# Kernel tuning notes

Measured on AMD Instinct MI355X. Metric: run time of the kernel, lower is better.

The kernel has to match this reference:

```python
import jax, jax.numpy as jnp
import numpy as np

B, LT, LC, D, H = 128, 64, 400, 768, 3072  # batch, template len, search len, dim, mlp hidden
NEG = -1e20


def _l2norm(x):
    # F.normalize(dim=-1): x / max(||x||, eps)
    n = jnp.sqrt(jnp.sum(x * x, axis=-1, keepdims=True))
    return x / jnp.maximum(n, 1e-12)


def setup_inputs() -> dict:
    key = jax.random.key(0)
    ks = jax.random.split(key, 10)
    tem = jax.random.normal(ks[0], (B, LT, D), jnp.float32)
    ctx = jax.random.normal(ks[1], (B, LC, D), jnp.float32)
    cls_token = jax.random.normal(ks[2], (B, D), jnp.float32)
    tem_mask = jax.random.randint(ks[3], (B, LT), 0, 2) > 0
    ctx_mask = jax.random.randint(ks[4], (B, LC), 0, 2) > 0
    flag = jax.random.randint(ks[5], (B,), 0, 3)
    query_embed = jax.random.normal(ks[6], (3, D), jnp.float32) * 0.02
    logit_scale = jnp.asarray(np.log(1.0 / 0.07), jnp.float32)
    fc1_w = jax.random.normal(ks[7], (D, H), jnp.float32) * 0.02
    fc1_b = jnp.zeros((H,), jnp.float32)
    fc2_w = jax.random.normal(ks[8], (H, D), jnp.float32) * 0.02
    fc2_b = jnp.zeros((D,), jnp.float32)
    return dict(tem=tem, tem_mask=tem_mask, ctx=ctx, ctx_mask=ctx_mask,
                cls_token=cls_token, flag=flag, query_embed=query_embed,
                logit_scale=logit_scale, fc1_w=fc1_w, fc1_b=fc1_b,
                fc2_w=fc2_w, fc2_b=fc2_b)


def _divide_background(bgd_score):
    # sort ascending, cumsum threshold at 0.25, keep scores >= threshold
    values = jnp.sort(bgd_score, axis=-1)
    mask = jnp.cumsum(values, axis=-1) < 0.25
    threshold = jnp.min(jnp.where(mask, 1.0, values), axis=-1, keepdims=True)
    return bgd_score >= threshold


def _forward(tem, ctx, cls_token, query_embed, logit_scale,
             fc1_w, fc1_b, fc2_w, fc2_b, tem_mask, ctx_mask, flag):
    b = tem.shape[0]
    src_ = jnp.tile(query_embed[None], (b, 1, 1)).at[:, 0].add(cls_token)  # [B,3,D]
    tgt = jnp.concatenate([tem, ctx], axis=1)                               # [B,L,D]
    tgt_mask = jnp.concatenate([tem_mask, ctx_mask], axis=1)[:, None, :]    # [B,1,L]
    sim_logit = jnp.einsum('bd,bld->bl', _l2norm(cls_token), _l2norm(tgt))[:, None, :]
    sim_logit = sim_logit * jnp.exp(logit_scale)                            # [B,1,L]

    tgt_score = jax.nn.softmax(jnp.where(tgt_mask, sim_logit, NEG), axis=-1)
    tgt_token = tgt_score @ tgt                                             # [B,1,D]
    bgd_logit = jnp.where(tgt_mask, NEG, sim_logit)
    bgd_score0 = jax.nn.softmax(bgd_logit, axis=-1)
    dis_mask = _divide_background(bgd_score0)
    bgd_score = jax.nn.softmax(jnp.where(dis_mask, NEG, bgd_logit), axis=-1)
    dis_score = jax.nn.softmax(jnp.where(dis_mask, bgd_logit, NEG), axis=-1)
    bgd_token = bgd_score @ tgt
    dis_token = dis_score @ tgt

    src = jnp.concatenate([tgt_token, dis_token, bgd_token], axis=1) + src_  # [B,3,D]
    h = jax.nn.gelu(src @ fc1_w + fc1_b, approximate=False)
    src = (h @ fc2_w + fc2_b) + src
    # stack [src, src_, src] and pick per-sample by flag
    stacked = jnp.stack([src, src_, src], axis=1)                            # [B,3,3,D]
    out = jnp.take_along_axis(stacked, flag[:, None, None, None], axis=1)[:, 0]
    return out  # [B,3,D]


def reference(tem, tem_mask, ctx, ctx_mask, cls_token, flag, query_embed,
              logit_scale, fc1_w, fc1_b, fc2_w, fc2_b):
    return _forward(tem, ctx, cls_token, query_embed, logit_scale,
                    fc1_w, fc1_b, fc2_w, fc2_b, tem_mask, ctx_mask, flag)
```

## Files before the change

kernel.cpp:

```cpp
#include <hip/hip_runtime.h>
#include <hip/hip_bf16.h>
#include <math.h>

typedef unsigned short u16;
typedef unsigned int   u32;
typedef unsigned char  u8;

#define NB  128
#define NLT 64
#define NLC 400
#define NL  464
#define ND  768
#define NH  3072
#define NEGF (-1e20f)

typedef __attribute__((ext_vector_type(8))) short bf16x8;
typedef __attribute__((ext_vector_type(4))) float f32x4;

__device__ __forceinline__ float b2f(u16 u){ return __uint_as_float(((u32)u)<<16); }
__device__ __forceinline__ u16 f2b(float f){
  u32 x = __float_as_uint(f);
  x += 0x7fffu + ((x>>16)&1u);
  return (u16)(x>>16);
}
template<bool BF> __device__ __forceinline__ float ldf(const void* p, size_t i){
  if constexpr (BF) return b2f(((const u16*)p)[i]);
  else              return ((const float*)p)[i];
}

__device__ __forceinline__ void detect_inline(const void* tem, const void* tmask,
                                              int* sh2, int& bf, int& m8){
  int tid = threadIdx.x;
  if (tid < 64){
    const u16* p = (const u16*)tem;
    float acc = 0.f;
    for (int i = tid; i < 512; i += 64){
      float v = fabsf(b2f(p[i]));
      acc += fminf(v, 1e10f);
    }
    for (int o = 32; o; o >>= 1) acc += __shfl_down(acc, o);
    const u8* mb = (const u8*)tmask;
    int nz = 0;
    for (int i = tid; i < 400; i += 64) if ((i & 3) != 0 && mb[i] != 0) nz = 1;
    unsigned long long anym = __ballot(nz);
    if (tid == 0){ sh2[0] = (acc < 1e4f) ? 1 : 0; sh2[1] = anym ? 1 : 0; }
  }
  __syncthreads();
  bf = sh2[0]; m8 = sh2[1];
}

__global__ __launch_bounds__(256) void k_prep(const void* tem, const void* tmask,
    const void* w1, const void* w2, u16* __restrict__ w1t, u16* __restrict__ w2t,
    int* flags){
  __shared__ int sh2[2];
  __shared__ u16 tile[64][66];
  int bf, m8;
  detect_inline(tem, tmask, sh2, bf, m8);
  if (blockIdx.x == 0 && blockIdx.y == 0 && threadIdx.x == 0){
    flags[0] = bf; flags[1] = m8;
  }
  int which = blockIdx.y;
  const void* W = which ? w2 : w1;
  u16* Wt = which ? w2t : w1t;
  int K = which ? NH : ND;
  int N = which ? ND : NH;
  int nt = N >> 6;
  int tk = blockIdx.x / nt, tn = blockIdx.x - tk*nt;
  int k0 = tk*64, n0 = tn*64;
  int r = threadIdx.x >> 6, c = threadIdx.x & 63;
  #pragma unroll
  for (int i = 0; i < 16; i++){
    int row = i*4 + r;
    size_t idx = (size_t)(k0 + row)*N + n0 + c;
    tile[row][c] = bf ? ((const u16*)W)[idx] : f2b(((const float*)W)[idx]);
  }
  __syncthreads();
  #pragma unroll
  for (int i = 0; i < 16; i++){
    int nrow = i*4 + r;
    Wt[(size_t)(n0 + nrow)*K + k0 + c] = tile[c][nrow];
  }
}

template<bool BF>
__device__ void sim_body(const void* tem, const void* ctx, const void* cls,
                         const void* lsp, float* sim,
                         float* clsf, float* red4, float* cnorm)
{
  int b = blockIdx.x, tile = blockIdx.y, tid = threadIdx.x;
  for (int i = tid; i < ND; i += 256) clsf[i] = ldf<BF>(cls, (size_t)b*ND + i);
  __syncthreads();
  float ss = 0.f;
  for (int i = tid; i < ND; i += 256) ss += clsf[i]*clsf[i];
  for (int off = 32; off; off >>= 1) ss += __shfl_down(ss, off);
  if ((tid & 63) == 0) red4[tid >> 6] = ss;
  __syncthreads();
  if (tid == 0) *cnorm = fmaxf(sqrtf(red4[0]+red4[1]+red4[2]+red4[3]), 1e-12f);
  __syncthreads();
  float cn = *cnorm;
  float escale = expf(ldf<BF>(lsp, 0));
  int lane = tid & 63, w = tid >> 6;
  float creg[12];
  #pragma unroll
  for (int j = 0; j < 12; j++) creg[j] = clsf[lane*12 + j];

  for (int rr = 0; rr < 4; rr++){
    int l = tile*16 + w + rr*4;
    float v[12];
    if constexpr (BF){
      const u16* row = (l < NLT) ? ((const u16*)tem + ((size_t)b*NLT + l)*ND)
                                 : ((const u16*)ctx + ((size_t)b*NLC + (l-NLT))*ND);
      const ushort4* rp = (const ushort4*)(row + lane*12);
      #pragma unroll
      for (int q = 0; q < 3; q++){
        ushort4 u = rp[q];
        v[q*4+0]=b2f(u.x); v[q*4+1]=b2f(u.y); v[q*4+2]=b2f(u.z); v[q*4+3]=b2f(u.w);
      }
    } else {
      const float* row = (l < NLT) ? ((const float*)tem + ((size_t)b*NLT + l)*ND)
                                   : ((const float*)ctx + ((size_t)b*NLC + (l-NLT))*ND);
      const float4* rp = (const float4*)(row + lane*12);
      #pragma unroll
      for (int q = 0; q < 3; q++){
        float4 u = rp[q];
        v[q*4+0]=u.x; v[q*4+1]=u.y; v[q*4+2]=u.z; v[q*4+3]=u.w;
      }
    }
    float dot = 0.f, rs = 0.f;
    #pragma unroll
    for (int j = 0; j < 12; j++){ dot += creg[j]*v[j]; rs += v[j]*v[j]; }
    for (int off = 32; off; off >>= 1){
      dot += __shfl_down(dot, off); rs += __shfl_down(rs, off);
    }
    if (lane == 0){
      float rn = fmaxf(sqrtf(rs), 1e-12f);
      sim[(size_t)b*NL + l] = dot / (cn*rn) * escale;
    }
  }
}
__global__ __launch_bounds__(256) void k_sim(const int* flags, const void* tem,
    const void* ctx, const void* cls, const void* lsp, float* sim){
  __shared__ float clsf[ND];
  __shared__ float red4[4];
  __shared__ float cnorm;
  if (flags[0]) sim_body<true >(tem, ctx, cls, lsp, sim, clsf, red4, &cnorm);
  else          sim_body<false>(tem, ctx, cls, lsp, sim, clsf, red4, &cnorm);
}

__device__ __forceinline__ float bsum512(float v, float* l8, int tid){
  #pragma unroll
  for (int o = 32; o; o >>= 1) v += __shfl_xor(v, o);
  __syncthreads();
  if ((tid & 63) == 0) l8[tid >> 6] = v;
  __syncthreads();
  float s = l8[0];
  #pragma unroll
  for (int i = 1; i < 8; i++) s += l8[i];
  return s;
}
__device__ __forceinline__ float bmax512(float v, float* l8, int tid){
  #pragma unroll
  for (int o = 32; o; o >>= 1) v = fmaxf(v, __shfl_xor(v, o));
  __syncthreads();
  if ((tid & 63) == 0) l8[tid >> 6] = v;
  __syncthreads();
  float s = l8[0];
  #pragma unroll
  for (int i = 1; i < 8; i++) s = fmaxf(s, l8[i]);
  return s;
}
__device__ __forceinline__ float bmin512(float v, float* l8, int tid){
  #pragma unroll
  for (int o = 32; o; o >>= 1) v = fminf(v, __shfl_xor(v, o));
  __syncthreads();
  if ((tid & 63) == 0) l8[tid >> 6] = v;
  __syncthreads();
  float s = l8[0];
  #pragma unroll
  for (int i = 1; i < 8; i++) s = fminf(s, l8[i]);
  return s;
}

template<bool M8>
__device__ void scores_body(const float* sim, const void* tmask, const void* cmask,
                            float* tgts, float* diss, float* bgds,
                            float* srt, float* wsum, float* l8)
{
  int b = blockIdx.x, tid = threadIdx.x;
  int lane = tid & 63, wid = tid >> 6;
  bool valid = tid < NL;
  float sv = valid ? sim[(size_t)b*NL + tid] : 0.f;
  bool mk = false;
  if (valid){
    if constexpr (M8)
      mk = (tid < NLT) ? (((const u8*)tmask)[b*NLT + tid] != 0)
                       : (((const u8*)cmask)[b*NLC + tid - NLT] != 0);
    else
      mk = (tid < NLT) ? (((const int*)tmask)[b*NLT + tid] != 0)
                       : (((const int*)cmask)[b*NLC + tid - NLT] != 0);
  }
  float lt = (valid && mk) ? sv : NEGF;
  float m1 = bmax512(lt, l8, tid);
  float e1 = valid ? expf(lt - m1) : 0.f;
  float s1 = bsum512(e1, l8, tid);
  if (valid) tgts[(size_t)b*NL + tid] = e1/s1;

  float bl = (valid && !mk) ? sv : NEGF;
  float m2 = bmax512(bl, l8, tid);
  float e2 = valid ? expf(bl - m2) : 0.f;
  float s2 = bsum512(e2, l8, tid);
  float bg0 = e2/s2;

  float v = valid ? bg0 : INFINITY;
  for (int k = 2; k <= 512; k <<= 1){
    for (int j = k >> 1; j >= 64; j >>= 1){
      __syncthreads();
      srt[tid] = v;
      __syncthreads();
      float p = srt[tid ^ j];
      bool up = ((tid & k) == 0), lower = ((tid & j) == 0);
      v = (up == lower) ? fminf(v, p) : fmaxf(v, p);
    }
    int j0 = (k >> 1) < 32 ? (k >> 1) : 32;
    for (int j = j0; j >= 1; j >>= 1){
      float p = __shfl_xor(v, j);
      bool up = ((tid & k) == 0), lower = ((tid & j) == 0);
      v = (up == lower) ? fminf(v, p) : fmaxf(v, p);
    }
  }
  float c = v;
  #pragma unroll
  for (int o = 1; o < 64; o <<= 1){
    float t = __shfl_up(c, o);
    if (lane >= o) c += t;
  }
  __syncthreads();
  if (lane == 63) wsum[wid] = c;
  __syncthreads();
  float off = 0.f;
  for (int i = 0; i < wid; i++) off += wsum[i];
  c += off;
  float cand = (c < 0.25f) ? 1.0f : v;
  float thr = bmin512(cand, l8, tid);

  bool dm = valid && (bg0 >= thr);
  float dl = dm ? bl : NEGF;
  float l2 = dm ? NEGF : bl;
  float m3 = bmax512(dl, l8, tid);
  float e3 = valid ? expf(dl - m3) : 0.f;
  float s3 = bsum512(e3, l8, tid);
  if (valid) diss[(size_t)b*NL + tid] = e3/s3;
  float m4 = bmax512(l2, l8, tid);
  float e4 = valid ? expf(l2 - m4) : 0.f;
  float s4 = bsum512(e4, l8, tid);
  if (valid) bgds[(size_t)b*NL + tid] = e4/s4;
}
__global__ __launch_bounds__(512) void k_scores(const int* flags, const float* sim,
    const void* tmask, const void* cmask, float* tgts, float* diss, float* bgds){
  __shared__ float srt[512];
  __shared__ float wsum[8];
  __shared__ float l8[8];
  if (flags[1]) scores_body<true >(sim, tmask, cmask, tgts, diss, bgds, srt, wsum, l8);
  else          scores_body<false>(sim, tmask, cmask, tgts, diss, bgds, srt, wsum, l8);
}

template<bool BF>
__device__ void tok_body(const void* tem, const void* ctx, const void* cls, const void* qe,
                         const float* __restrict__ tgts, const float* __restrict__ diss,
                         const float* __restrict__ bgds,
                         float* __restrict__ src0f, u16* __restrict__ src0b,
                         float (*ws)[NL], float (*red)[3][264])
{
  int b = blockIdx.x, dc = blockIdx.y, tid = threadIdx.x;
  int g = tid >> 5, l32 = tid & 31;
  int c0 = dc*256 + l32*8;
  for (int i = tid; i < NL; i += 256){
    ws[0][i] = tgts[(size_t)b*NL + i];
    ws[1][i] = diss[(size_t)b*NL + i];
    ws[2][i] = bgds[(size_t)b*NL + i];
  }
  __syncthreads();
  float acc[3][8];
  #pragma unroll
  for (int j = 0; j < 3; j++)
    #pragma unroll
    for (int q = 0; q < 8; q++) acc[j][q] = 0.f;

  for (int it = 0; it < 58; it++){
    int l = it*8 + g;
    float f[8];
    if constexpr (BF){
      const u16* row = (l < NLT) ? ((const u16*)tem + ((size_t)b*NLT + l)*ND)
                                 : ((const u16*)ctx + ((size_t)b*NLC + (l-NLT))*ND);
      uint4 v = *(const uint4*)(row + c0);
      f[0]=b2f((u16)(v.x&0xffff)); f[1]=b2f((u16)(v.x>>16));
      f[2]=b2f((u16)(v.y&0xffff)); f[3]=b2f((u16)(v.y>>16));
      f[4]=b2f((u16)(v.z&0xffff)); f[5]=b2f((u16)(v.z>>16));
      f[6]=b2f((u16)(v.w&0xffff)); f[7]=b2f((u16)(v.w>>16));
    } else {
      const float* row = (l < NLT) ? ((const float*)tem + ((size_t)b*NLT + l)*ND)
                                   : ((const float*)ctx + ((size_t)b*NLC + (l-NLT))*ND);
      float4 v0 = *(const float4*)(row + c0);
      float4 v1 = *(const float4*)(row + c0 + 4);
      f[0]=v0.x; f[1]=v0.y; f[2]=v0.z; f[3]=v0.w;
      f[4]=v1.x; f[5]=v1.y; f[6]=v1.z; f[7]=v1.w;
    }
    float w0 = ws[0][l], w1 = ws[1][l], w2 = ws[2][l];
    #pragma unroll
    for (int q = 0; q < 8; q++){
      acc[0][q] = fmaf(w0, f[q], acc[0][q]);
      acc[1][q] = fmaf(w1, f[q], acc[1][q]);
      acc[2][q] = fmaf(w2, f[q], acc[2][q]);
    }
  }
  #pragma unroll
  for (int j = 0; j < 3; j++)
    #pragma unroll
    for (int q = 0; q < 8; q++) red[g][j][l32*8 + q] = acc[j][q];
  __syncthreads();
  int col = dc*256 + tid;
  #pragma unroll
  for (int j = 0; j < 3; j++){
    float s = 0.f;
    #pragma unroll
    for (int g2 = 0; g2 < 8; g2++) s += red[g2][j][tid];
    s += ldf<BF>(qe, (size_t)j*ND + col);
    if (j == 0) s += ldf<BF>(cls, (size_t)b*ND + col);
    size_t oi = ((size_t)b*3 + j)*ND + col;
    src0f[oi] = s;
    src0b[oi] = f2b(s);
  }
}
__global__ __launch_bounds__(256) void k_tok(const int* flags, const void* tem,
    const void* ctx, const void* cls, const void* qe,
    const float* tgts, const float* diss, const float* bgds,
    float* src0f, u16* src0b){
  __shared__ float ws[3][NL];
  __shared__ float red[8][3][264];
  if (flags[0]) tok_body<true >(tem, ctx, cls, qe, tgts, diss, bgds, src0f, src0b, ws, red);
  else          tok_body<false>(tem, ctx, cls, qe, tgts, diss, bgds, src0f, src0b, ws, red);
}

__device__ __forceinline__ void mfma_loop2(const u16* __restrict__ A, int lda,
                                           const u16* __restrict__ B, int ldb,
                                           int m0, int n0, int kb_, int ke_,
                                           u16* lds, f32x4 (&acc)[2][2])
{
  int tid = threadIdx.x, lane = tid & 63;
  int w = tid >> 6, wr = w >> 1, wc = w & 1;
  #pragma unroll
  for (int i = 0; i < 2; i++)
    #pragma unroll
    for (int j = 0; j < 2; j++) acc[i][j] = (f32x4){0.f,0.f,0.f,0.f};

  int rS = tid >> 2, kcS = (tid & 3) * 16;
  uint4 a0, a1, b0, b1;
  auto LOAD = [&](int k0){
    const uint4* pa = (const uint4*)(A + (size_t)(m0 + rS)*lda + k0 + kcS);
    a0 = pa[0]; a1 = pa[1];
    const uint4* pb = (const uint4*)(B + (size_t)(n0 + rS)*ldb + k0 + kcS);
    b0 = pb[0]; b1 = pb[1];
  };
  auto WRITE = [&](u16* L){
    u32 sw = (u32)((rS & 7) << 4);
    u32 ba = (u32)(rS*128 + kcS*2);
    *(uint4*)((char*)L + (ba ^ sw)) = a0;
    *(uint4*)((char*)L + ((ba + 16) ^ sw)) = a1;
    *(uint4*)((char*)L + 8192 + (ba ^ sw)) = b0;
    *(uint4*)((char*)L + 8192 + ((ba + 16) ^ sw)) = b1;
  };

  int nt = (ke_ - kb_) >> 6;
  LOAD(kb_);
  WRITE(lds);
  __syncthreads();
  int cur = 0;
  for (int t = 0; t < nt; t++){
    if (t + 1 < nt) LOAD(kb_ + (t+1)*64);
    u16* L = lds + (size_t)cur*8192;
    #pragma unroll
    for (int kb = 0; kb < 2; kb++){
      bf16x8 af[2], bfr[2];
      #pragma unroll
      for (int i = 0; i < 2; i++){
        int ml = wr*32 + i*16 + (lane & 15);
        u32 ab = (u32)(ml*128 + kb*64 + (lane >> 4)*16) ^ (u32)((ml & 7) << 4);
        af[i] = *(const bf16x8*)((char*)L + ab);
        int cl = wc*32 + i*16 + (lane & 15);
        u32 bb = (u32)(cl*128 + kb*64 + (lane >> 4)*16) ^ (u32)((cl & 7) << 4);
        bfr[i] = *(const bf16x8*)((char*)L + 8192 + bb);
      }
      #pragma unroll
      for (int i = 0; i < 2; i++)
        #pragma unroll
        for (int j = 0; j < 2; j++)
          acc[i][j] = __builtin_amdgcn_mfma_f32_16x16x32_bf16(af[i], bfr[j], acc[i][j], 0, 0, 0);
    }
    if (t + 1 < nt) WRITE(lds + (size_t)(cur^1)*8192);
    __syncthreads();
    cur ^= 1;
  }
}

template<bool BF>
__device__ void fc1_body(const u16* src0b, const u16* w1t, const void* b1, u16* hbf, u16* lds){
  int n0 = blockIdx.x*64, m0 = blockIdx.y*64;
  f32x4 acc[2][2];
  mfma_loop2(src0b, ND, w1t, ND, m0, n0, 0, ND, lds, acc);
  int lane = threadIdx.x & 63, w = threadIdx.x >> 6, wr = w >> 1, wc = w & 1;
  #pragma unroll
  for (int j = 0; j < 2; j++){
    int n = n0 + wc*32 + j*16 + (lane & 15);
    float bb = ldf<BF>(b1, n);
    #pragma unroll
    for (int i = 0; i < 2; i++){
      int mb = m0 + wr*32 + i*16 + (lane >> 4)*4;
      #pragma unroll
      for (int r = 0; r < 4; r++){
        float x = acc[i][j][r] + bb;
        float g = 0.5f*x*(1.0f + erff(x*0.70710678118654752f));
        hbf[(size_t)(mb + r)*NH + n] = f2b(g);
      }
    }
  }
}
__global__ __launch_bounds__(256) void k_fc1(const int* flags, const u16* src0b,
    const u16* w1t, const void* b1, u16* hbf){
  __shared__ u16 lds[16384];
  if (flags[0]) fc1_body<true >(src0b, w1t, b1, hbf, lds);
  else          fc1_body<false>(src0b, w1t, b1, hbf, lds);
}

__global__ __launch_bounds__(256) void k_fc2(const int* flags, const u16* hbf,
    const u16* w2t, float* fc2p){
  __shared__ u16 lds[16384];
  int n0 = blockIdx.x*64, m0 = blockIdx.y*64, z = blockIdx.z;
  f32x4 acc[2][2];
  mfma_loop2(hbf, NH, w2t, NH, m0, n0, z*768, (z+1)*768, lds, acc);
  int lane = threadIdx.x & 63, w = threadIdx.x >> 6, wr = w >> 1, wc = w & 1;
  float* po = fc2p + (size_t)z*(384*ND);
  #pragma unroll
  for (int j = 0; j < 2; j++){
    int n = n0 + wc*32 + j*16 + (lane & 15);
    #pragma unroll
    for (int i = 0; i < 2; i++){
      int mb = m0 + wr*32 + i*16 + (lane >> 4)*4;
      #pragma unroll
      for (int r = 0; r < 4; r++)
        po[(size_t)(mb + r)*ND + n] = acc[i][j][r];
    }
  }
}

template<bool BF>
__device__ void fin_body(const float* __restrict__ p, const void* b2,
                         const float* __restrict__ src0f, const void* cls,
                         const void* qe, const int* flag, void* out){
  int idx = (blockIdx.x*256 + threadIdx.x)*4;
  int r = idx / ND;
  int n = idx % ND;
  float s[4] = {0,0,0,0};
  #pragma unroll
  for (int ksp = 0; ksp < 4; ksp++){
    float4 v = *(const float4*)(p + (size_t)ksp*(384*ND) + idx);
    s[0]+=v.x; s[1]+=v.y; s[2]+=v.z; s[3]+=v.w;
  }
  float4 res = *(const float4*)(src0f + idx);
  const float* rp = &res.x;
  int bi = r/3, j = r - bi*3;
  bool take_src_ = (flag[bi] == 1);
  #pragma unroll
  for (int jj = 0; jj < 4; jj++){
    float val = s[jj] + ldf<BF>(b2, n + jj) + rp[jj];
    if (take_src_){
      val = ldf<BF>(qe, (size_t)j*ND + n + jj)
          + ((j == 0) ? ldf<BF>(cls, (size_t)bi*ND + n + jj) : 0.f);
    }
    s[jj] = val;
  }
  if constexpr (BF){
    ushort4 o = { f2b(s[0]), f2b(s[1]), f2b(s[2]), f2b(s[3]) };
    *(ushort4*)((u16*)out + idx) = o;
  } else {
    float4 o = {s[0], s[1], s[2], s[3]};
    *(float4*)((float*)out + idx) = o;
  }
}
__global__ __launch_bounds__(256) void k_fin(const int* flags, const float* p,
    const void* b2, const float* src0f, const void* cls, const void* qe,
    const int* flag, void* out){
  if (flags[0]) fin_body<true >(p, b2, src0f, cls, qe, flag, out);
  else          fin_body<false>(p, b2, src0f, cls, qe, flag, out);
}

extern "C" void kernel_launch(void* const* d_in, const int* in_sizes, int n_in,
                              void* d_out, int out_size, void* d_ws, size_t ws_size,
                              hipStream_t stream)
{
  const void* tem   = d_in[0];
  const void* tmask = d_in[1];
  const void* ctx   = d_in[2];
  const void* cmask = d_in[3];
  const void* cls   = d_in[4];
  const int*  flag  = (const int*)d_in[5];
  const void* qe    = d_in[6];
  const void* ls    = d_in[7];
  const void* w1    = d_in[8];
  const void* b1    = d_in[9];
  const void* w2    = d_in[10];
  const void* b2    = d_in[11];

  int*   flags = (int*)d_ws;
  float* p     = (float*)d_ws + 16;
  float* sim   = p;  p += (size_t)NB*NL;
  float* tgts  = p;  p += (size_t)NB*NL;
  float* diss  = p;  p += (size_t)NB*NL;
  float* bgds  = p;  p += (size_t)NB*NL;
  float* src0f = p;  p += (size_t)384*ND;
  u16*   src0b = (u16*)p; p += (size_t)384*ND/2;
  u16*   hbf   = (u16*)p; p += (size_t)384*NH/2;
  float* fc2p  = p;  p += (size_t)4*384*ND;
  u16*   w1t   = (u16*)p; p += (size_t)ND*NH/2;
  u16*   w2t   = (u16*)p; p += (size_t)ND*NH/2;

  hipLaunchKernelGGL(k_prep,   dim3(576, 2), dim3(256), 0, stream,
                     tem, tmask, w1, w2, w1t, w2t, flags);
  hipLaunchKernelGGL(k_sim,    dim3(NB, 29), dim3(256), 0, stream, flags, tem, ctx, cls, ls, sim);
  hipLaunchKernelGGL(k_scores, dim3(NB), dim3(512), 0, stream, flags, sim, tmask, cmask, tgts, diss, bgds);
  hipLaunchKernelGGL(k_tok,    dim3(NB, 3), dim3(256), 0, stream,
                     flags, tem, ctx, cls, qe, tgts, diss, bgds, src0f, src0b);
  hipLaunchKernelGGL(k_fc1,    dim3(NH/64, 384/64), dim3(256), 0, stream, flags, src0b, w1t, b1, hbf);
  hipLaunchKernelGGL(k_fc2,    dim3(ND/64, 384/64, 4), dim3(256), 0, stream, flags, hbf, w2t, fc2p);
  hipLaunchKernelGGL(k_fin,    dim3(384*ND/1024), dim3(256), 0, stream,
                     flags, fc2p, b2, src0f, cls, qe, flag, d_out);
}
```

Before: 106.9 us.

## Fuse weight prep into sim kernel and stage bf16 copy of tgt for token pass

Merges the weight-transpose kernel and the similarity kernel into one launch with a flat grid, so both run concurrently and one launch is saved. In the fp32 path, the similarity pass also writes a bf16 copy of the concatenated tem/ctx rows, which the token-pooling kernel then reads instead of re-reading the fp32 inputs. This halves the bytes read in the token pass but adds an extra bf16 write of the whole tgt tensor and drops precision of the pooled tokens to bf16. The fused kernel also carries extra shared memory, which may lower occupancy.

```diff
diff --git a/kernel.cpp b/kernel.cpp
--- a/kernel.cpp
+++ b/kernel.cpp
@@ -49,45 +49,13 @@
   bf = sh2[0]; m8 = sh2[1];
 }
 
-__global__ __launch_bounds__(256) void k_prep(const void* tem, const void* tmask,
-    const void* w1, const void* w2, u16* __restrict__ w1t, u16* __restrict__ w2t,
-    int* flags){
-  __shared__ int sh2[2];
-  __shared__ u16 tile[64][66];
-  int bf, m8;
-  detect_inline(tem, tmask, sh2, bf, m8);
-  if (blockIdx.x == 0 && blockIdx.y == 0 && threadIdx.x == 0){
-    flags[0] = bf; flags[1] = m8;
-  }
-  int which = blockIdx.y;
-  const void* W = which ? w2 : w1;
-  u16* Wt = which ? w2t : w1t;
-  int K = which ? NH : ND;
-  int N = which ? ND : NH;
-  int nt = N >> 6;
-  int tk = blockIdx.x / nt, tn = blockIdx.x - tk*nt;
-  int k0 = tk*64, n0 = tn*64;
-  int r = threadIdx.x >> 6, c = threadIdx.x & 63;
-  #pragma unroll
-  for (int i = 0; i < 16; i++){
-    int row = i*4 + r;
-    size_t idx = (size_t)(k0 + row)*N + n0 + c;
-    tile[row][c] = bf ? ((const u16*)W)[idx] : f2b(((const float*)W)[idx]);
-  }
-  __syncthreads();
-  #pragma unroll
-  for (int i = 0; i < 16; i++){
-    int nrow = i*4 + r;
-    Wt[(size_t)(n0 + nrow)*K + k0 + c] = tile[c][nrow];
-  }
-}
-
 template<bool BF>
 __device__ void sim_body(const void* tem, const void* ctx, const void* cls,
-                         const void* lsp, float* sim,
+                         const void* lsp, float* sim, u16* __restrict__ tgtb,
+                         int b, int tile,
                          float* clsf, float* red4, float* cnorm)
 {
-  int b = blockIdx.x, tile = blockIdx.y, tid = threadIdx.x;
+  int tid = threadIdx.x;
   for (int i = tid; i < ND; i += 256) clsf[i] = ldf<BF>(cls, (size_t)b*ND + i);
   __syncthreads();
   float ss = 0.f;
@@ -125,6 +93,13 @@
         float4 u = rp[q];
         v[q*4+0]=u.x; v[q*4+1]=u.y; v[q*4+2]=u.z; v[q*4+3]=u.w;
       }
+      u16* orow = tgtb + ((size_t)b*NL + l)*ND + lane*12;
+      ushort4 s0 = { f2b(v[0]), f2b(v[1]), f2b(v[2]),  f2b(v[3]) };
+      ushort4 s1 = { f2b(v[4]), f2b(v[5]), f2b(v[6]),  f2b(v[7]) };
+      ushort4 s2 = { f2b(v[8]), f2b(v[9]), f2b(v[10]), f2b(v[11]) };
+      *(ushort4*)(orow + 0) = s0;
+      *(ushort4*)(orow + 4) = s1;
+      *(ushort4*)(orow + 8) = s2;
     }
     float dot = 0.f, rs = 0.f;
     #pragma unroll
@@ -138,13 +113,51 @@
     }
   }
 }
-__global__ __launch_bounds__(256) void k_sim(const int* flags, const void* tem,
-    const void* ctx, const void* cls, const void* lsp, float* sim){
+
+__global__ __launch_bounds__(256) void k_presim(const void* tem, const void* tmask,
+    const void* ctx, const void* cls, const void* lsp,
+    const void* w1, const void* w2, u16* __restrict__ w1t, u16* __restrict__ w2t,
+    float* sim, u16* tgtb, int* flags)
+{
+  __shared__ int sh2[2];
+  __shared__ u16 tile[64][66];
   __shared__ float clsf[ND];
   __shared__ float red4[4];
   __shared__ float cnorm;
-  if (flags[0]) sim_body<true >(tem, ctx, cls, lsp, sim, clsf, red4, &cnorm);
-  else          sim_body<false>(tem, ctx, cls, lsp, sim, clsf, red4, &cnorm);
+  int bf, m8;
+  detect_inline(tem, tmask, sh2, bf, m8);
+  int bid = blockIdx.x;
+  if (bid == 0 && threadIdx.x == 0){ flags[0] = bf; flags[1] = m8; }
+
+  if (bid < 1152){
+    int which = (bid >= 576) ? 1 : 0;
+    int t = which ? bid - 576 : bid;
+    const void* W = which ? w2 : w1;
+    u16* Wt = which ? w2t : w1t;
+    int K = which ? NH : ND;
+    int N = which ? ND : NH;
+    int nt = N >> 6;
+    int tk = t / nt, tn = t - tk*nt;
+    int k0 = tk*64, n0 = tn*64;
+    int r = threadIdx.x >> 6, c = threadIdx.x & 63;
+    #pragma unroll
+    for (int i = 0; i < 16; i++){
+      int row = i*4 + r;
+      size_t idx = (size_t)(k0 + row)*N + n0 + c;
+      tile[row][c] = bf ? ((const u16*)W)[idx] : f2b(((const float*)W)[idx]);
+    }
+    __syncthreads();
+    #pragma unroll
+    for (int i = 0; i < 16; i++){
+      int nrow = i*4 + r;
+      Wt[(size_t)(n0 + nrow)*K + k0 + c] = tile[c][nrow];
+    }
+  } else {
+    int sid = bid - 1152;
+    int b = sid / 29, tl = sid - b*29;
+    if (bf) sim_body<true >(tem, ctx, cls, lsp, sim, tgtb, b, tl, clsf, red4, &cnorm);
+    else    sim_body<false>(tem, ctx, cls, lsp, sim, tgtb, b, tl, clsf, red4, &cnorm);
+  }
 }
 
 __device__ __forceinline__ float bsum512(float v, float* l8, int tid){
@@ -265,7 +278,8 @@
 }
 
 template<bool BF>
-__device__ void tok_body(const void* tem, const void* ctx, const void* cls, const void* qe,
+__device__ void tok_body(const void* tem, const void* ctx, const u16* __restrict__ tgtb,
+                         const void* cls, const void* qe,
                          const float* __restrict__ tgts, const float* __restrict__ diss,
                          const float* __restrict__ bgds,
                          float* __restrict__ src0f, u16* __restrict__ src0b,
@@ -288,23 +302,19 @@
 
   for (int it = 0; it < 58; it++){
     int l = it*8 + g;
+    const u16* row;
+    if constexpr (BF){
+      row = (l < NLT) ? ((const u16*)tem + ((size_t)b*NLT + l)*ND)
+                      : ((const u16*)ctx + ((size_t)b*NLC + (l-NLT))*ND);
+    } else {
+      row = tgtb + ((size_t)b*NL + l)*ND;
+    }
+    uint4 v = *(const uint4*)(row + c0);
     float f[8];
-    if constexpr (BF){
-      const u16* row = (l < NLT) ? ((const u16*)tem + ((size_t)b*NLT + l)*ND)
-                                 : ((const u16*)ctx + ((size_t)b*NLC + (l-NLT))*ND);
-      uint4 v = *(const uint4*)(row + c0);
-      f[0]=b2f((u16)(v.x&0xffff)); f[1]=b2f((u16)(v.x>>16));
-      f[2]=b2f((u16)(v.y&0xffff)); f[3]=b2f((u16)(v.y>>16));
-      f[4]=b2f((u16)(v.z&0xffff)); f[5]=b2f((u16)(v.z>>16));
-      f[6]=b2f((u16)(v.w&0xffff)); f[7]=b2f((u16)(v.w>>16));
-    } else {
-      const float* row = (l < NLT) ? ((const float*)tem + ((size_t)b*NLT + l)*ND)
-                                   : ((const float*)ctx + ((size_t)b*NLC + (l-NLT))*ND);
-      float4 v0 = *(const float4*)(row + c0);
-      float4 v1 = *(const float4*)(row + c0 + 4);
-      f[0]=v0.x; f[1]=v0.y; f[2]=v0.z; f[3]=v0.w;
-      f[4]=v1.x; f[5]=v1.y; f[6]=v1.z; f[7]=v1.w;
-    }
+    f[0]=b2f((u16)(v.x&0xffff)); f[1]=b2f((u16)(v.x>>16));
+    f[2]=b2f((u16)(v.y&0xffff)); f[3]=b2f((u16)(v.y>>16));
+    f[4]=b2f((u16)(v.z&0xffff)); f[5]=b2f((u16)(v.z>>16));
+    f[6]=b2f((u16)(v.w&0xffff)); f[7]=b2f((u16)(v.w>>16));
     float w0 = ws[0][l], w1 = ws[1][l], w2 = ws[2][l];
     #pragma unroll
     for (int q = 0; q < 8; q++){
@@ -332,13 +342,13 @@
   }
 }
 __global__ __launch_bounds__(256) void k_tok(const int* flags, const void* tem,
-    const void* ctx, const void* cls, const void* qe,
+    const void* ctx, const u16* tgtb, const void* cls, const void* qe,
     const float* tgts, const float* diss, const float* bgds,
     float* src0f, u16* src0b){
   __shared__ float ws[3][NL];
   __shared__ float red[8][3][264];
-  if (flags[0]) tok_body<true >(tem, ctx, cls, qe, tgts, diss, bgds, src0f, src0b, ws, red);
-  else          tok_body<false>(tem, ctx, cls, qe, tgts, diss, bgds, src0f, src0b, ws, red);
+  if (flags[0]) tok_body<true >(tem, ctx, tgtb, cls, qe, tgts, diss, bgds, src0f, src0b, ws, red);
+  else          tok_body<false>(tem, ctx, tgtb, cls, qe, tgts, diss, bgds, src0f, src0b, ws, red);
 }
 
 __device__ __forceinline__ void mfma_loop2(const u16* __restrict__ A, int lda,
@@ -522,13 +532,13 @@
   float* fc2p  = p;  p += (size_t)4*384*ND;
   u16*   w1t   = (u16*)p; p += (size_t)ND*NH/2;
   u16*   w2t   = (u16*)p; p += (size_t)ND*NH/2;
-
-  hipLaunchKernelGGL(k_prep,   dim3(576, 2), dim3(256), 0, stream,
-                     tem, tmask, w1, w2, w1t, w2t, flags);
-  hipLaunchKernelGGL(k_sim,    dim3(NB, 29), dim3(256), 0, stream, flags, tem, ctx, cls, ls, sim);
+  u16*   tgtb  = (u16*)p; p += (size_t)NB*NL*ND/2;
+
+  hipLaunchKernelGGL(k_presim, dim3(1152 + NB*29), dim3(256), 0, stream,
+                     tem, tmask, ctx, cls, ls, w1, w2, w1t, w2t, sim, tgtb, flags);
   hipLaunchKernelGGL(k_scores, dim3(NB), dim3(512), 0, stream, flags, sim, tmask, cmask, tgts, diss, bgds);
   hipLaunchKernelGGL(k_tok,    dim3(NB, 3), dim3(256), 0, stream,
-                     flags, tem, ctx, cls, qe, tgts, diss, bgds, src0f, src0b);
+                     flags, tem, ctx, tgtb, cls, qe, tgts, diss, bgds, src0f, src0b);
   hipLaunchKernelGGL(k_fc1,    dim3(NH/64, 384/64), dim3(256), 0, stream, flags, src0b, w1t, b1, hbf);
   hipLaunchKernelGGL(k_fc2,    dim3(ND/64, 384/64, 4), dim3(256), 0, stream, flags, hbf, w2t, fc2p);
   hipLaunchKernelGGL(k_fin,    dim3(384*ND/1024), dim3(256), 0, stream,
```

Measured after the change: 115.8 us. 8.2% more time.

## Fuse weight-transpose prep and similarity kernels into one launch

Applied to the files above, without the earlier changes.

Merges the weight transpose/convert kernel and the cosine-similarity kernel into a single launch, with the first 256 blocks computing similarities and the rest transposing weights. This removes one kernel launch and lets the two independent jobs run concurrently. The similarity computation is also restructured so each thread computes a full row dot product with vectorized loads instead of a wave-wide shuffle reduction. The trade-off is fewer blocks (256) for the sim work, each thread streaming an entire 768-element row, which may hurt memory coalescing.

```diff
diff --git a/kernel.cpp b/kernel.cpp
--- a/kernel.cpp
+++ b/kernel.cpp
@@ -49,102 +49,116 @@
   bf = sh2[0]; m8 = sh2[1];
 }
 
-__global__ __launch_bounds__(256) void k_prep(const void* tem, const void* tmask,
+template<bool BF>
+__device__ void sim_body(const void* tem, const void* ctx, const void* cls,
+                         const void* lsp, float* sim, int b, int h,
+                         float* clsf, float* l4)
+{
+  int tid = threadIdx.x;
+  for (int i = tid; i < ND; i += 256) clsf[i] = ldf<BF>(cls, (size_t)b*ND + i);
+  __syncthreads();
+  float ss = 0.f;
+  for (int i = tid; i < ND; i += 256) ss += clsf[i]*clsf[i];
+  #pragma unroll
+  for (int o = 32; o; o >>= 1) ss += __shfl_xor(ss, o);
+  if ((tid & 63) == 0) l4[tid >> 6] = ss;
+  __syncthreads();
+  float cn = fmaxf(sqrtf(l4[0]+l4[1]+l4[2]+l4[3]), 1e-12f);
+  float escale = expf(ldf<BF>(lsp, 0));
+
+  if (tid >= 232) return;
+  int l = h*232 + tid;
+  float d0=0,d1=0,d2=0,d3=0, s0=0,s1=0,s2=0,s3=0;
+  const float4* c4 = (const float4*)clsf;
+
+  if constexpr (BF){
+    const u16* row = (l < NLT) ? ((const u16*)tem + ((size_t)b*NLT + l)*ND)
+                               : ((const u16*)ctx + ((size_t)b*NLC + (l-NLT))*ND);
+    const uint4* r8 = (const uint4*)row;
+    for (int k = 0; k < 96; k += 16){
+      #pragma unroll
+      for (int q = 0; q < 16; q++){
+        uint4 rv = r8[k+q];
+        float4 ca = c4[(k+q)*2], cb = c4[(k+q)*2+1];
+        float f0=b2f((u16)(rv.x&0xffff)), f1=b2f((u16)(rv.x>>16));
+        float f2=b2f((u16)(rv.y&0xffff)), f3=b2f((u16)(rv.y>>16));
+        float f4=b2f((u16)(rv.z&0xffff)), f5=b2f((u16)(rv.z>>16));
+        float f6=b2f((u16)(rv.w&0xffff)), f7=b2f((u16)(rv.w>>16));
+        d0=fmaf(f0,ca.x,d0); s0=fmaf(f0,f0,s0);
+        d1=fmaf(f1,ca.y,d1); s1=fmaf(f1,f1,s1);
+        d2=fmaf(f2,ca.z,d2); s2=fmaf(f2,f2,s2);
+        d3=fmaf(f3,ca.w,d3); s3=fmaf(f3,f3,s3);
+        d0=fmaf(f4,cb.x,d0); s0=fmaf(f4,f4,s0);
+        d1=fmaf(f5,cb.y,d1); s1=fmaf(f5,f5,s1);
+        d2=fmaf(f6,cb.z,d2); s2=fmaf(f6,f6,s2);
+        d3=fmaf(f7,cb.w,d3); s3=fmaf(f7,f7,s3);
+      }
+    }
+  } else {
+    const float* row = (l < NLT) ? ((const float*)tem + ((size_t)b*NLT + l)*ND)
+                                 : ((const float*)ctx + ((size_t)b*NLC + (l-NLT))*ND);
+    const float4* r4 = (const float4*)row;
+    for (int k = 0; k < 192; k += 16){
+      #pragma unroll
+      for (int q = 0; q < 16; q++){
+        float4 rv = r4[k+q];
+        float4 cv = c4[k+q];
+        d0=fmaf(rv.x,cv.x,d0); s0=fmaf(rv.x,rv.x,s0);
+        d1=fmaf(rv.y,cv.y,d1); s1=fmaf(rv.y,rv.y,s1);
+        d2=fmaf(rv.z,cv.z,d2); s2=fmaf(rv.z,rv.z,s2);
+        d3=fmaf(rv.w,cv.w,d3); s3=fmaf(rv.w,rv.w,s3);
+      }
+    }
+  }
+  float dot = (d0+d1)+(d2+d3);
+  float rs  = (s0+s1)+(s2+s3);
+  float rn = fmaxf(sqrtf(rs), 1e-12f);
+  sim[(size_t)b*NL + l] = dot/(cn*rn)*escale;
+}
+
+__global__ __launch_bounds__(256) void k_presim(const void* tem, const void* tmask,
+    const void* ctx, const void* cls, const void* lsp,
     const void* w1, const void* w2, u16* __restrict__ w1t, u16* __restrict__ w2t,
-    int* flags){
+    float* sim, int* flags)
+{
   __shared__ int sh2[2];
   __shared__ u16 tile[64][66];
+  __shared__ float clsf[ND];
+  __shared__ float l4[4];
   int bf, m8;
   detect_inline(tem, tmask, sh2, bf, m8);
-  if (blockIdx.x == 0 && blockIdx.y == 0 && threadIdx.x == 0){
-    flags[0] = bf; flags[1] = m8;
-  }
-  int which = blockIdx.y;
-  const void* W = which ? w2 : w1;
-  u16* Wt = which ? w2t : w1t;
-  int K = which ? NH : ND;
-  int N = which ? ND : NH;
-  int nt = N >> 6;
-  int tk = blockIdx.x / nt, tn = blockIdx.x - tk*nt;
-  int k0 = tk*64, n0 = tn*64;
-  int r = threadIdx.x >> 6, c = threadIdx.x & 63;
-  #pragma unroll
-  for (int i = 0; i < 16; i++){
-    int row = i*4 + r;
-    size_t idx = (size_t)(k0 + row)*N + n0 + c;
-    tile[row][c] = bf ? ((const u16*)W)[idx] : f2b(((const float*)W)[idx]);
-  }
-  __syncthreads();
-  #pragma unroll
-  for (int i = 0; i < 16; i++){
-    int nrow = i*4 + r;
-    Wt[(size_t)(n0 + nrow)*K + k0 + c] = tile[c][nrow];
-  }
-}
-
-template<bool BF>
-__device__ void sim_body(const void* tem, const void* ctx, const void* cls,
-                         const void* lsp, float* sim,
-                         float* clsf, float* red4, float* cnorm)
-{
-  int b = blockIdx.x, tile = blockIdx.y, tid = threadIdx.x;
-  for (int i = tid; i < ND; i += 256) clsf[i] = ldf<BF>(cls, (size_t)b*ND + i);
-  __syncthreads();
-  float ss = 0.f;
-  for (int i = tid; i < ND; i += 256) ss += clsf[i]*clsf[i];
-  for (int off = 32; off; off >>= 1) ss += __shfl_down(ss, off);
-  if ((tid & 63) == 0) red4[tid >> 6] = ss;
-  __syncthreads();
-  if (tid == 0) *cnorm = fmaxf(sqrtf(red4[0]+red4[1]+red4[2]+red4[3]), 1e-12f);
-  __syncthreads();
-  float cn = *cnorm;
-  float escale = expf(ldf<BF>(lsp, 0));
-  int lane = tid & 63, w = tid >> 6;
-  float creg[12];
-  #pragma unroll
-  for (int j = 0; j < 12; j++) creg[j] = clsf[lane*12 + j];
-
-  for (int rr = 0; rr < 4; rr++){
-    int l = tile*16 + w + rr*4;
-    float v[12];
-    if constexpr (BF){
-      const u16* row = (l < NLT) ? ((const u16*)tem + ((size_t)b*NLT + l)*ND)
-                                 : ((const u16*)ctx + ((size_t)b*NLC + (l-NLT))*ND);
-      const ushort4* rp = (const ushort4*)(row + lane*12);
-      #pragma unroll
-      for (int q = 0; q < 3; q++){
-        ushort4 u = rp[q];
-        v[q*4+0]=b2f(u.x); v[q*4+1]=b2f(u.y); v[q*4+2]=b2f(u.z); v[q*4+3]=b2f(u.w);
-      }
-    } else {
-      const float* row = (l < NLT) ? ((const float*)tem + ((size_t)b*NLT + l)*ND)
-                                   : ((const float*)ctx + ((size_t)b*NLC + (l-NLT))*ND);
-      const float4* rp = (const float4*)(row + lane*12);
-      #pragma unroll
-      for (int q = 0; q < 3; q++){
-        float4 u = rp[q];
-        v[q*4+0]=u.x; v[q*4+1]=u.y; v[q*4+2]=u.z; v[q*4+3]=u.w;
-      }
-    }
-    float dot = 0.f, rs = 0.f;
-    #pragma unroll
-    for (int j = 0; j < 12; j++){ dot += creg[j]*v[j]; rs += v[j]*v[j]; }
-    for (int off = 32; off; off >>= 1){
-      dot += __shfl_down(dot, off); rs += __shfl_down(rs, off);
-    }
-    if (lane == 0){
-      float rn = fmaxf(sqrtf(rs), 1e-12f);
-      sim[(size_t)b*NL + l] = dot / (cn*rn) * escale;
-    }
-  }
-}
-__global__ __launch_bounds__(256) void k_sim(const int* flags, const void* tem,
-    const void* ctx, const void* cls, const void* lsp, float* sim){
-  __shared__ float clsf[ND];
-  __shared__ float red4[4];
-  __shared__ float cnorm;
-  if (flags[0]) sim_body<true >(tem, ctx, cls, lsp, sim, clsf, red4, &cnorm);
-  else          sim_body<false>(tem, ctx, cls, lsp, sim, clsf, red4, &cnorm);
+  int bid = blockIdx.x;
+  if (bid == 0 && threadIdx.x == 0){ flags[0] = bf; flags[1] = m8; }
+
+  if (bid < 256){
+    int b = bid >> 1, h = bid & 1;
+    if (bf) sim_body<true >(tem, ctx, cls, lsp, sim, b, h, clsf, l4);
+    else    sim_body<false>(tem, ctx, cls, lsp, sim, b, h, clsf, l4);
+  } else {
+    int t = bid - 256;
+    int which = (t >= 576) ? 1 : 0;
+    if (which) t -= 576;
+    const void* W = which ? w2 : w1;
+    u16* Wt = which ? w2t : w1t;
+    int K = which ? NH : ND;
+    int N = which ? ND : NH;
+    int nt = N >> 6;
+    int tk = t / nt, tn = t - tk*nt;
+    int k0 = tk*64, n0 = tn*64;
+    int r = threadIdx.x >> 6, c = threadIdx.x & 63;
+    #pragma unroll
+    for (int i = 0; i < 16; i++){
+      int row = i*4 + r;
+      size_t idx = (size_t)(k0 + row)*N + n0 + c;
+      tile[row][c] = bf ? ((const u16*)W)[idx] : f2b(((const float*)W)[idx]);
+    }
+    __syncthreads();
+    #pragma unroll
+    for (int i = 0; i < 16; i++){
+      int nrow = i*4 + r;
+      Wt[(size_t)(n0 + nrow)*K + k0 + c] = tile[c][nrow];
+    }
+  }
 }
 
 __device__ __forceinline__ float bsum512(float v, float* l8, int tid){
@@ -523,9 +537,8 @@
   u16*   w1t   = (u16*)p; p += (size_t)ND*NH/2;
   u16*   w2t   = (u16*)p; p += (size_t)ND*NH/2;
 
-  hipLaunchKernelGGL(k_prep,   dim3(576, 2), dim3(256), 0, stream,
-                     tem, tmask, w1, w2, w1t, w2t, flags);
-  hipLaunchKernelGGL(k_sim,    dim3(NB, 29), dim3(256), 0, stream, flags, tem, ctx, cls, ls, sim);
+  hipLaunchKernelGGL(k_presim, dim3(256 + 1152), dim3(256), 0, stream,
+                     tem, tmask, ctx, cls, ls, w1, w2, w1t, w2t, sim, flags);
   hipLaunchKernelGGL(k_scores, dim3(NB), dim3(512), 0, stream, flags, sim, tmask, cmask, tgts, diss, bgds);
   hipLaunchKernelGGL(k_tok,    dim3(NB, 3), dim3(256), 0, stream,
                      flags, tem, ctx, cls, qe, tgts, diss, bgds, src0f, src0b);
```

New measurement: 104.1 us. 1.03x faster.
